# Kernel optimization log

Hardware: AMD Instinct MI355X
Metric: run time of the kernel (lower is better)

The kernel has to match this reference:

```python
import jax, jax.numpy as jnp
import numpy as np

N = 100000   # nodes
E = 1600000  # edges (avg degree 16)
IN, HID, OUT = 128, 128, 40
EPS = 1e-5   # BatchNorm1d default eps


def _lin(k, fan_in, fan_out):
    # Glorot-ish init for the linear weights
    return jax.random.normal(k, (fan_in, fan_out), jnp.float32) / np.sqrt(fan_in).astype(np.float32)


def setup_inputs() -> dict:
    key = jax.random.key(0)
    ks = jax.random.split(key, 12)
    return {
        "x": jax.random.normal(ks[0], (N, IN), jnp.float32),
        "edge_src": jax.random.randint(ks[1], (E,), 0, N, jnp.int32),
        "edge_dst": jax.random.randint(ks[2], (E,), 0, N, jnp.int32),
        # layer 0 (SAGEConv in->hid): lin_l (with bias) on aggregated neighbors, lin_r (no bias) on root
        "W_l0": _lin(ks[3], IN, HID), "b_l0": jnp.zeros((HID,), jnp.float32), "W_r0": _lin(ks[4], IN, HID),
        "g0": jnp.ones((HID,), jnp.float32), "be0": jnp.zeros((HID,), jnp.float32),
        # layer 1 (SAGEConv hid->hid)
        "W_l1": _lin(ks[5], HID, HID), "b_l1": jnp.zeros((HID,), jnp.float32), "W_r1": _lin(ks[6], HID, HID),
        "g1": jnp.ones((HID,), jnp.float32), "be1": jnp.zeros((HID,), jnp.float32),
        # layer 2 (SAGEConv hid->out)
        "W_l2": _lin(ks[7], HID, OUT), "b_l2": jnp.zeros((OUT,), jnp.float32), "W_r2": _lin(ks[8], HID, OUT),
    }


def reference(x, edge_src, edge_dst,
              W_l0, b_l0, W_r0, g0, be0,
              W_l1, b_l1, W_r1, g1, be1,
              W_l2, b_l2, W_r2):
    deg = jax.ops.segment_sum(jnp.ones((E,), x.dtype), edge_dst, num_segments=N)
    inv_deg = 1.0 / jnp.maximum(deg, 1.0)  # [N]

    def sage_conv(h, Wl, bl, Wr):
        # mean aggregation of neighbor features (gather + scatter-add), then two linears
        agg = jax.ops.segment_sum(h[edge_src], edge_dst, num_segments=N) * inv_deg[:, None]
        return agg @ Wl + bl + h @ Wr

    def bn(h, g, b):
        # BatchNorm1d in training mode: batch statistics over the node dimension
        m = h.mean(axis=0)
        v = h.var(axis=0)
        return (h - m) * (g / jnp.sqrt(v + EPS)) + b

    h = jax.nn.relu(bn(sage_conv(x, W_l0, b_l0, W_r0), g0, be0))
    h = jax.nn.relu(bn(sage_conv(h, W_l1, b_l1, W_r1), g1, be1))
    h = sage_conv(h, W_l2, b_l2, W_r2)
    return jax.nn.log_softmax(h, axis=-1)
```

## Files before the change

kernel.cpp:

```cpp
#include <hip/hip_runtime.h>
#include <hip/hip_bf16.h>

#define NNODES 100000
#define NEDGES 1600000
#define CH 128
#define OUTC 40
#define BN_EPS 1e-5f

__global__ void k_deg(const int* __restrict__ dst, int* __restrict__ deg) {
    int e = blockIdx.x * blockDim.x + threadIdx.x;
    if (e < NEDGES) atomicAdd(&deg[dst[e]], 1);
}

__global__ void k_scan1(const int* __restrict__ deg, int* __restrict__ row_ptr,
                        int* __restrict__ blkSums, float* __restrict__ inv_deg) {
    __shared__ int sd[256];
    int base = blockIdx.x * 1024 + threadIdx.x * 4;
    int t[4];
#pragma unroll
    for (int j = 0; j < 4; ++j) {
        int i = base + j;
        t[j] = (i < NNODES) ? deg[i] : 0;
        if (i < NNODES) inv_deg[i] = 1.0f / fmaxf((float)t[j], 1.0f);
    }
    int tsum = t[0] + t[1] + t[2] + t[3];
    sd[threadIdx.x] = tsum;
    __syncthreads();
    for (int off = 1; off < 256; off <<= 1) {
        int v = (threadIdx.x >= off) ? sd[threadIdx.x - off] : 0;
        __syncthreads();
        sd[threadIdx.x] += v;
        __syncthreads();
    }
    int run = sd[threadIdx.x] - tsum;
#pragma unroll
    for (int j = 0; j < 4; ++j) {
        int i = base + j;
        if (i < NNODES) row_ptr[i] = run;
        run += t[j];
    }
    if (threadIdx.x == 255) blkSums[blockIdx.x] = sd[255];
}

__global__ void k_scan2(int* blkSums, int nb) {
    if (threadIdx.x == 0 && blockIdx.x == 0) {
        int run = 0;
        for (int b = 0; b < nb; ++b) { int v = blkSums[b]; blkSums[b] = run; run += v; }
    }
}

__global__ void k_scan3(int* __restrict__ row_ptr, int* __restrict__ cursor,
                        const int* __restrict__ blkSums) {
    int i = blockIdx.x * blockDim.x + threadIdx.x;
    if (i < NNODES) {
        int v = row_ptr[i] + blkSums[i >> 10];
        row_ptr[i] = v;
        cursor[i] = v;
    }
    if (i == 0) row_ptr[NNODES] = NEDGES;
}

__global__ void k_fill(const int* __restrict__ src, const int* __restrict__ dst,
                       int* __restrict__ cursor, int* __restrict__ sorted_src) {
    int e = blockIdx.x * blockDim.x + threadIdx.x;
    if (e < NEDGES) {
        int d = dst[e];
        int pos = atomicAdd(&cursor[d], 1);
        sorted_src[pos] = src[e];
    }
}

template <bool BN>
__global__ void k_aggregate(const float* __restrict__ h, const int* __restrict__ row_ptr,
                            const int* __restrict__ sorted_src, const float* __restrict__ inv_deg,
                            const float* __restrict__ bnscale, const float* __restrict__ bnshift,
                            float* __restrict__ agg) {
    int wave = threadIdx.x >> 6;
    int lane = threadIdx.x & 63;
    int node = blockIdx.x * 4 + wave;
    if (node >= NNODES) return;
    float2 sc = make_float2(1.f, 1.f), sh = make_float2(0.f, 0.f);
    if (BN) {
        sc = *(const float2*)&bnscale[lane * 2];
        sh = *(const float2*)&bnshift[lane * 2];
    }
    int s0 = row_ptr[node], s1 = row_ptr[node + 1];
    float ax = 0.f, ay = 0.f;
    const float2* hp = (const float2*)h;
    for (int e = s0; e < s1; ++e) {
        int s = sorted_src[e];
        float2 v = hp[(size_t)s * 64 + lane];
        if (BN) {
            v.x = fmaxf(fmaf(v.x, sc.x, sh.x), 0.f);
            v.y = fmaxf(fmaf(v.y, sc.y, sh.y), 0.f);
        }
        ax += v.x; ay += v.y;
    }
    float w = inv_deg[node];
    float2* ap = (float2*)agg;
    ap[(size_t)node * 64 + lane] = make_float2(ax * w, ay * w);
}

template <int NC, int WPAD, bool BN_A, bool STATS, bool LSM>
__global__ __launch_bounds__(256) void k_gemm(
    const float* __restrict__ agg, const float* __restrict__ hin,
    const float* __restrict__ Wl, const float* __restrict__ Wr,
    const float* __restrict__ bias,
    const float* __restrict__ bnscale, const float* __restrict__ bnshift,
    float* __restrict__ z, float* __restrict__ sums) {
    constexpr int CPT = (NC + 15) / 16;
    __shared__ float A_lds[128 * 36];
    __shared__ float W_lds[32 * WPAD];
    int tid = threadIdx.x;
    int ty = tid >> 4, tx = tid & 15;
    int row0 = blockIdx.x * 128;
    float acc[8][CPT];
#pragma unroll
    for (int i = 0; i < 8; ++i)
#pragma unroll
        for (int j = 0; j < CPT; ++j) acc[i][j] = 0.f;

    for (int half = 0; half < 2; ++half) {
        const float* Asrc = half ? hin : agg;
        const float* Wsrc = half ? Wr : Wl;
        for (int kc = 0; kc < CH; kc += 32) {
            __syncthreads();
#pragma unroll
            for (int q = 0; q < 4; ++q) {
                int r = (tid >> 3) + 32 * q;
                int c = (tid & 7) << 2;
                int gr = row0 + r;
                float4 v = make_float4(0.f, 0.f, 0.f, 0.f);
                if (gr < NNODES) v = *(const float4*)&Asrc[(size_t)gr * CH + kc + c];
                if (BN_A && half == 1) {
                    float4 s4 = *(const float4*)&bnscale[kc + c];
                    float4 h4 = *(const float4*)&bnshift[kc + c];
                    v.x = fmaxf(fmaf(v.x, s4.x, h4.x), 0.f);
                    v.y = fmaxf(fmaf(v.y, s4.y, h4.y), 0.f);
                    v.z = fmaxf(fmaf(v.z, s4.z, h4.z), 0.f);
                    v.w = fmaxf(fmaf(v.w, s4.w, h4.w), 0.f);
                }
                *(float4*)&A_lds[r * 36 + c] = v;
            }
            for (int idx = tid; idx < 32 * WPAD; idx += 256) {
                int k = idx / WPAD, c = idx - k * WPAD;
                W_lds[idx] = (c < NC) ? Wsrc[(kc + k) * NC + c] : 0.f;
            }
            __syncthreads();
#pragma unroll 8
            for (int k = 0; k < 32; ++k) {
                float a[8];
#pragma unroll
                for (int i = 0; i < 8; ++i) a[i] = A_lds[(ty + 16 * i) * 36 + k];
                float wv[CPT];
#pragma unroll
                for (int j = 0; j < CPT; ++j) wv[j] = W_lds[k * WPAD + tx + 16 * j];
#pragma unroll
                for (int i = 0; i < 8; ++i)
#pragma unroll
                    for (int j = 0; j < CPT; ++j) acc[i][j] = fmaf(a[i], wv[j], acc[i][j]);
            }
        }
    }

    float bcol[CPT];
#pragma unroll
    for (int j = 0; j < CPT; ++j) {
        int c = tx + 16 * j;
        bcol[j] = (c < NC) ? bias[c] : 0.f;
    }
#pragma unroll
    for (int i = 0; i < 8; ++i)
#pragma unroll
        for (int j = 0; j < CPT; ++j) acc[i][j] += bcol[j];

    if (!LSM) {
#pragma unroll
        for (int i = 0; i < 8; ++i) {
            int gr = row0 + ty + 16 * i;
            if (gr >= NNODES) continue;
#pragma unroll
            for (int j = 0; j < CPT; ++j) {
                int c = tx + 16 * j;
                if (c < NC) z[(size_t)gr * NC + c] = acc[i][j];
            }
        }
    }

    if (STATS) {
        __shared__ float smem_s[4][128];
        __shared__ float smem_q[4][128];
        float s[CPT], q[CPT];
#pragma unroll
        for (int j = 0; j < CPT; ++j) { s[j] = 0.f; q[j] = 0.f; }
#pragma unroll
        for (int i = 0; i < 8; ++i) {
            int gr = row0 + ty + 16 * i;
            if (gr < NNODES) {
#pragma unroll
                for (int j = 0; j < CPT; ++j) {
                    float a = acc[i][j];
                    s[j] += a; q[j] += a * a;
                }
            }
        }
#pragma unroll
        for (int j = 0; j < CPT; ++j) {
            s[j] += __shfl_xor(s[j], 16); q[j] += __shfl_xor(q[j], 16);
            s[j] += __shfl_xor(s[j], 32); q[j] += __shfl_xor(q[j], 32);
        }
        int wv = tid >> 6, lane = tid & 63;
        if (lane < 16) {
#pragma unroll
            for (int j = 0; j < CPT; ++j) {
                smem_s[wv][lane + 16 * j] = s[j];
                smem_q[wv][lane + 16 * j] = q[j];
            }
        }
        __syncthreads();
        if (tid < NC) {
            atomicAdd(&sums[tid], smem_s[0][tid] + smem_s[1][tid] + smem_s[2][tid] + smem_s[3][tid]);
        } else if (tid >= 128 && tid < 128 + NC) {
            int c = tid - 128;
            atomicAdd(&sums[128 + c], smem_q[0][c] + smem_q[1][c] + smem_q[2][c] + smem_q[3][c]);
        }
    }

    if (LSM) {
#pragma unroll
        for (int i = 0; i < 8; ++i) {
            int gr = row0 + ty + 16 * i;
            if (gr >= NNODES) continue;
            float m = -INFINITY;
#pragma unroll
            for (int j = 0; j < CPT; ++j)
                if (tx + 16 * j < NC) m = fmaxf(m, acc[i][j]);
            m = fmaxf(m, __shfl_xor(m, 1));
            m = fmaxf(m, __shfl_xor(m, 2));
            m = fmaxf(m, __shfl_xor(m, 4));
            m = fmaxf(m, __shfl_xor(m, 8));
            float se = 0.f;
#pragma unroll
            for (int j = 0; j < CPT; ++j)
                if (tx + 16 * j < NC) se += expf(acc[i][j] - m);
            se += __shfl_xor(se, 1);
            se += __shfl_xor(se, 2);
            se += __shfl_xor(se, 4);
            se += __shfl_xor(se, 8);
            float lse = m + logf(se);
#pragma unroll
            for (int j = 0; j < CPT; ++j) {
                int c = tx + 16 * j;
                if (c < NC) z[(size_t)gr * NC + c] = acc[i][j] - lse;
            }
        }
    }
}

__global__ void k_bn_finalize(const float* __restrict__ sums, const float* __restrict__ g,
                              const float* __restrict__ be, float* __restrict__ scale,
                              float* __restrict__ shift) {
    int c = threadIdx.x;
    if (c < CH) {
        float mean = sums[c] * (1.0f / NNODES);
        float var = sums[128 + c] * (1.0f / NNODES) - mean * mean;
        float sc = g[c] * rsqrtf(var + BN_EPS);
        scale[c] = sc;
        shift[c] = be[c] - mean * sc;
    }
}

extern "C" void kernel_launch(void* const* d_in, const int* in_sizes, int n_in,
                              void* d_out, int out_size, void* d_ws, size_t ws_size,
                              hipStream_t stream) {
    const float* x   = (const float*)d_in[0];
    const int* esrc  = (const int*)d_in[1];
    const int* edst  = (const int*)d_in[2];
    const float* W_l0 = (const float*)d_in[3];
    const float* b_l0 = (const float*)d_in[4];
    const float* W_r0 = (const float*)d_in[5];
    const float* g0   = (const float*)d_in[6];
    const float* be0  = (const float*)d_in[7];
    const float* W_l1 = (const float*)d_in[8];
    const float* b_l1 = (const float*)d_in[9];
    const float* W_r1 = (const float*)d_in[10];
    const float* g1   = (const float*)d_in[11];
    const float* be1  = (const float*)d_in[12];
    const float* W_l2 = (const float*)d_in[13];
    const float* b_l2 = (const float*)d_in[14];
    const float* W_r2 = (const float*)d_in[15];
    float* out = (float*)d_out;

    char* w = (char*)d_ws;
    size_t o = 0;
    auto nxt = [&](size_t b) { void* p = w + o; o = (o + b + 511) & ~(size_t)511; return p; };
    int* deg      = (int*)nxt((size_t)NNODES * 4);
    int* row_ptr  = (int*)nxt((size_t)(NNODES + 1) * 4);
    int* cursor   = (int*)nxt((size_t)NNODES * 4);
    float* invdeg = (float*)nxt((size_t)NNODES * 4);
    int* blkSums  = (int*)nxt(128 * 4);
    float* sums   = (float*)nxt(512 * 4);
    float* scsh   = (float*)nxt(512 * 4);
    int* sorted   = (int*)nxt((size_t)NEDGES * 4);
    float* agg    = (float*)nxt((size_t)NNODES * CH * 4);
    float* z0     = (float*)nxt((size_t)NNODES * CH * 4);
    float* z1     = (float*)nxt((size_t)NNODES * CH * 4);
    float* sums0 = sums, *sums1 = sums + 256;
    float* scale0 = scsh, *shift0 = scsh + 128, *scale1 = scsh + 256, *shift1 = scsh + 384;

    hipMemsetAsync(deg, 0, (size_t)NNODES * 4, stream);
    hipMemsetAsync(sums, 0, 512 * 4, stream);

    const int EB = (NEDGES + 255) / 256;
    const int SCAN_B = (NNODES + 1023) / 1024;
    const int NB = (NNODES + 255) / 256;
    const int AGG_B = (NNODES + 3) / 4;
    const int GEMM_B = (NNODES + 127) / 128;

    k_deg<<<EB, 256, 0, stream>>>(edst, deg);
    k_scan1<<<SCAN_B, 256, 0, stream>>>(deg, row_ptr, blkSums, invdeg);
    k_scan2<<<1, 64, 0, stream>>>(blkSums, SCAN_B);
    k_scan3<<<NB, 256, 0, stream>>>(row_ptr, cursor, blkSums);
    k_fill<<<EB, 256, 0, stream>>>(esrc, edst, cursor, sorted);

    k_aggregate<false><<<AGG_B, 256, 0, stream>>>(x, row_ptr, sorted, invdeg,
                                                  nullptr, nullptr, agg);
    k_gemm<128, 132, false, true, false><<<GEMM_B, 256, 0, stream>>>(
        agg, x, W_l0, W_r0, b_l0, nullptr, nullptr, z0, sums0);
    k_bn_finalize<<<1, 128, 0, stream>>>(sums0, g0, be0, scale0, shift0);

    k_aggregate<true><<<AGG_B, 256, 0, stream>>>(z0, row_ptr, sorted, invdeg,
                                                 scale0, shift0, agg);
    k_gemm<128, 132, true, true, false><<<GEMM_B, 256, 0, stream>>>(
        agg, z0, W_l1, W_r1, b_l1, scale0, shift0, z1, sums1);
    k_bn_finalize<<<1, 128, 0, stream>>>(sums1, g1, be1, scale1, shift1);

    k_aggregate<true><<<AGG_B, 256, 0, stream>>>(z1, row_ptr, sorted, invdeg,
                                                 scale1, shift1, agg);
    k_gemm<40, 48, true, false, true><<<GEMM_B, 256, 0, stream>>>(
        agg, z1, W_l2, W_r2, b_l2, scale1, shift1, out, nullptr);
}
```

Baseline: 1.258 ms.

## Transform-then-aggregate: apply linear before mean aggregation, fuse combine with log-softmax

```diff
diff --git a/kernel.cpp b/kernel.cpp
--- a/kernel.cpp
+++ b/kernel.cpp
@@ -70,59 +70,29 @@
     }
 }
 
-template <bool BN>
-__global__ void k_aggregate(const float* __restrict__ h, const int* __restrict__ row_ptr,
-                            const int* __restrict__ sorted_src, const float* __restrict__ inv_deg,
-                            const float* __restrict__ bnscale, const float* __restrict__ bnshift,
-                            float* __restrict__ agg) {
-    int wave = threadIdx.x >> 6;
-    int lane = threadIdx.x & 63;
-    int node = blockIdx.x * 4 + wave;
-    if (node >= NNODES) return;
-    float2 sc = make_float2(1.f, 1.f), sh = make_float2(0.f, 0.f);
-    if (BN) {
-        sc = *(const float2*)&bnscale[lane * 2];
-        sh = *(const float2*)&bnshift[lane * 2];
-    }
-    int s0 = row_ptr[node], s1 = row_ptr[node + 1];
-    float ax = 0.f, ay = 0.f;
-    const float2* hp = (const float2*)h;
-    for (int e = s0; e < s1; ++e) {
-        int s = sorted_src[e];
-        float2 v = hp[(size_t)s * 64 + lane];
-        if (BN) {
-            v.x = fmaxf(fmaf(v.x, sc.x, sh.x), 0.f);
-            v.y = fmaxf(fmaf(v.y, sc.y, sh.y), 0.f);
-        }
-        ax += v.x; ay += v.y;
-    }
-    float w = inv_deg[node];
-    float2* ap = (float2*)agg;
-    ap[(size_t)node * 64 + lane] = make_float2(ax * w, ay * w);
-}
-
-template <int NC, int WPAD, bool BN_A, bool STATS, bool LSM>
-__global__ __launch_bounds__(256) void k_gemm(
-    const float* __restrict__ agg, const float* __restrict__ hin,
+template <int NC, int WP, bool BN_A>
+__global__ __launch_bounds__(256) void k_gemm2(
+    const float* __restrict__ h,
     const float* __restrict__ Wl, const float* __restrict__ Wr,
     const float* __restrict__ bias,
     const float* __restrict__ bnscale, const float* __restrict__ bnshift,
-    float* __restrict__ z, float* __restrict__ sums) {
-    constexpr int CPT = (NC + 15) / 16;
+    float* __restrict__ yl, float* __restrict__ yr) {
+    constexpr int NG = (NC == 128) ? 2 : 1;
+    constexpr int WSLOTS = NC / 4;
     __shared__ float A_lds[128 * 36];
-    __shared__ float W_lds[32 * WPAD];
+    __shared__ float W_lds[32 * WP];
     int tid = threadIdx.x;
     int ty = tid >> 4, tx = tid & 15;
     int row0 = blockIdx.x * 128;
-    float acc[8][CPT];
-#pragma unroll
-    for (int i = 0; i < 8; ++i)
-#pragma unroll
-        for (int j = 0; j < CPT; ++j) acc[i][j] = 0.f;
 
     for (int half = 0; half < 2; ++half) {
-        const float* Asrc = half ? hin : agg;
-        const float* Wsrc = half ? Wr : Wl;
+        const float* W = half ? Wr : Wl;
+        float acc[8][NG * 4];
+#pragma unroll
+        for (int i = 0; i < 8; ++i)
+#pragma unroll
+            for (int j = 0; j < NG * 4; ++j) acc[i][j] = 0.f;
+
         for (int kc = 0; kc < CH; kc += 32) {
             __syncthreads();
 #pragma unroll
@@ -131,8 +101,8 @@
                 int c = (tid & 7) << 2;
                 int gr = row0 + r;
                 float4 v = make_float4(0.f, 0.f, 0.f, 0.f);
-                if (gr < NNODES) v = *(const float4*)&Asrc[(size_t)gr * CH + kc + c];
-                if (BN_A && half == 1) {
+                if (gr < NNODES) v = *(const float4*)&h[(size_t)gr * CH + kc + c];
+                if (BN_A) {
                     float4 s4 = *(const float4*)&bnscale[kc + c];
                     float4 h4 = *(const float4*)&bnshift[kc + c];
                     v.x = fmaxf(fmaf(v.x, s4.x, h4.x), 0.f);
@@ -142,118 +112,160 @@
                 }
                 *(float4*)&A_lds[r * 36 + c] = v;
             }
-            for (int idx = tid; idx < 32 * WPAD; idx += 256) {
-                int k = idx / WPAD, c = idx - k * WPAD;
-                W_lds[idx] = (c < NC) ? Wsrc[(kc + k) * NC + c] : 0.f;
+            for (int idx = tid; idx < 32 * WSLOTS; idx += 256) {
+                int k = idx / WSLOTS, s = idx - k * WSLOTS;
+                *(float4*)&W_lds[k * WP + s * 4] = *(const float4*)&W[(size_t)(kc + k) * NC + s * 4];
             }
             __syncthreads();
-#pragma unroll 8
-            for (int k = 0; k < 32; ++k) {
-                float a[8];
-#pragma unroll
-                for (int i = 0; i < 8; ++i) a[i] = A_lds[(ty + 16 * i) * 36 + k];
-                float wv[CPT];
-#pragma unroll
-                for (int j = 0; j < CPT; ++j) wv[j] = W_lds[k * WPAD + tx + 16 * j];
+#pragma unroll
+            for (int k4 = 0; k4 < 32; k4 += 4) {
+                float4 a4[8];
 #pragma unroll
                 for (int i = 0; i < 8; ++i)
-#pragma unroll
-                    for (int j = 0; j < CPT; ++j) acc[i][j] = fmaf(a[i], wv[j], acc[i][j]);
+                    a4[i] = *(const float4*)&A_lds[(ty + 16 * i) * 36 + k4];
+#pragma unroll
+                for (int kk = 0; kk < 4; ++kk) {
+                    float4 w0 = *(const float4*)&W_lds[(k4 + kk) * WP + tx * 4];
+                    float4 w1;
+                    if (NG == 2) w1 = *(const float4*)&W_lds[(k4 + kk) * WP + 64 + tx * 4];
+#pragma unroll
+                    for (int i = 0; i < 8; ++i) {
+                        float av = (&a4[i].x)[kk];
+                        acc[i][0] = fmaf(av, w0.x, acc[i][0]);
+                        acc[i][1] = fmaf(av, w0.y, acc[i][1]);
+                        acc[i][2] = fmaf(av, w0.z, acc[i][2]);
+                        acc[i][3] = fmaf(av, w0.w, acc[i][3]);
+                        if (NG == 2) {
+                            acc[i][4] = fmaf(av, w1.x, acc[i][4]);
+                            acc[i][5] = fmaf(av, w1.y, acc[i][5]);
+                            acc[i][6] = fmaf(av, w1.z, acc[i][6]);
+                            acc[i][7] = fmaf(av, w1.w, acc[i][7]);
+                        }
+                    }
+                }
             }
         }
-    }
-
-    float bcol[CPT];
-#pragma unroll
-    for (int j = 0; j < CPT; ++j) {
-        int c = tx + 16 * j;
-        bcol[j] = (c < NC) ? bias[c] : 0.f;
-    }
-#pragma unroll
-    for (int i = 0; i < 8; ++i)
-#pragma unroll
-        for (int j = 0; j < CPT; ++j) acc[i][j] += bcol[j];
-
-    if (!LSM) {
+        float* Y = half ? yr : yl;
+        bool colok = (NC != 40) || (tx < 10);
+        float4 b0 = make_float4(0.f, 0.f, 0.f, 0.f), b1 = b0;
+        if (half == 1 && colok) {
+            b0 = *(const float4*)&bias[tx * 4];
+            if (NG == 2) b1 = *(const float4*)&bias[64 + tx * 4];
+        }
 #pragma unroll
         for (int i = 0; i < 8; ++i) {
             int gr = row0 + ty + 16 * i;
-            if (gr >= NNODES) continue;
-#pragma unroll
-            for (int j = 0; j < CPT; ++j) {
-                int c = tx + 16 * j;
-                if (c < NC) z[(size_t)gr * NC + c] = acc[i][j];
+            if (gr >= NNODES || !colok) continue;
+            float4 v0 = make_float4(acc[i][0] + b0.x, acc[i][1] + b0.y,
+                                    acc[i][2] + b0.z, acc[i][3] + b0.w);
+            *(float4*)&Y[(size_t)gr * NC + tx * 4] = v0;
+            if (NG == 2) {
+                float4 v1 = make_float4(acc[i][4] + b1.x, acc[i][5] + b1.y,
+                                        acc[i][6] + b1.z, acc[i][7] + b1.w);
+                *(float4*)&Y[(size_t)gr * NC + 64 + tx * 4] = v1;
             }
         }
     }
-
-    if (STATS) {
-        __shared__ float smem_s[4][128];
-        __shared__ float smem_q[4][128];
-        float s[CPT], q[CPT];
-#pragma unroll
-        for (int j = 0; j < CPT; ++j) { s[j] = 0.f; q[j] = 0.f; }
-#pragma unroll
-        for (int i = 0; i < 8; ++i) {
-            int gr = row0 + ty + 16 * i;
-            if (gr < NNODES) {
-#pragma unroll
-                for (int j = 0; j < CPT; ++j) {
-                    float a = acc[i][j];
-                    s[j] += a; q[j] += a * a;
-                }
-            }
-        }
-#pragma unroll
-        for (int j = 0; j < CPT; ++j) {
-            s[j] += __shfl_xor(s[j], 16); q[j] += __shfl_xor(q[j], 16);
-            s[j] += __shfl_xor(s[j], 32); q[j] += __shfl_xor(q[j], 32);
-        }
-        int wv = tid >> 6, lane = tid & 63;
-        if (lane < 16) {
-#pragma unroll
-            for (int j = 0; j < CPT; ++j) {
-                smem_s[wv][lane + 16 * j] = s[j];
-                smem_q[wv][lane + 16 * j] = q[j];
-            }
-        }
-        __syncthreads();
-        if (tid < NC) {
-            atomicAdd(&sums[tid], smem_s[0][tid] + smem_s[1][tid] + smem_s[2][tid] + smem_s[3][tid]);
-        } else if (tid >= 128 && tid < 128 + NC) {
-            int c = tid - 128;
-            atomicAdd(&sums[128 + c], smem_q[0][c] + smem_q[1][c] + smem_q[2][c] + smem_q[3][c]);
-        }
-    }
-
-    if (LSM) {
-#pragma unroll
-        for (int i = 0; i < 8; ++i) {
-            int gr = row0 + ty + 16 * i;
-            if (gr >= NNODES) continue;
-            float m = -INFINITY;
-#pragma unroll
-            for (int j = 0; j < CPT; ++j)
-                if (tx + 16 * j < NC) m = fmaxf(m, acc[i][j]);
-            m = fmaxf(m, __shfl_xor(m, 1));
-            m = fmaxf(m, __shfl_xor(m, 2));
-            m = fmaxf(m, __shfl_xor(m, 4));
-            m = fmaxf(m, __shfl_xor(m, 8));
-            float se = 0.f;
-#pragma unroll
-            for (int j = 0; j < CPT; ++j)
-                if (tx + 16 * j < NC) se += expf(acc[i][j] - m);
-            se += __shfl_xor(se, 1);
-            se += __shfl_xor(se, 2);
-            se += __shfl_xor(se, 4);
-            se += __shfl_xor(se, 8);
-            float lse = m + logf(se);
-#pragma unroll
-            for (int j = 0; j < CPT; ++j) {
-                int c = tx + 16 * j;
-                if (c < NC) z[(size_t)gr * NC + c] = acc[i][j] - lse;
-            }
-        }
+}
+
+__global__ void k_combine128(const float* __restrict__ yl, const int* __restrict__ row_ptr,
+                             const int* __restrict__ sorted_src, const float* __restrict__ inv_deg,
+                             float* __restrict__ z) {
+    int wave = threadIdx.x >> 6, lane = threadIdx.x & 63;
+    int node = blockIdx.x * 4 + wave;
+    if (node >= NNODES) return;
+    int s0 = row_ptr[node], s1 = row_ptr[node + 1];
+    const float2* Y = (const float2*)yl;
+    float ax0 = 0.f, ay0 = 0.f, ax1 = 0.f, ay1 = 0.f;
+    float ax2 = 0.f, ay2 = 0.f, ax3 = 0.f, ay3 = 0.f;
+    int e = s0;
+    for (; e + 4 <= s1; e += 4) {
+        int i0 = sorted_src[e], i1 = sorted_src[e + 1];
+        int i2 = sorted_src[e + 2], i3 = sorted_src[e + 3];
+        float2 v0 = Y[(size_t)i0 * 64 + lane];
+        float2 v1 = Y[(size_t)i1 * 64 + lane];
+        float2 v2 = Y[(size_t)i2 * 64 + lane];
+        float2 v3 = Y[(size_t)i3 * 64 + lane];
+        ax0 += v0.x; ay0 += v0.y; ax1 += v1.x; ay1 += v1.y;
+        ax2 += v2.x; ay2 += v2.y; ax3 += v3.x; ay3 += v3.y;
+    }
+    for (; e < s1; ++e) {
+        int i = sorted_src[e];
+        float2 v = Y[(size_t)i * 64 + lane];
+        ax0 += v.x; ay0 += v.y;
+    }
+    float w = inv_deg[node];
+    float2* Z = (float2*)z;
+    float2 r = Z[(size_t)node * 64 + lane];
+    r.x += (ax0 + ax1 + ax2 + ax3) * w;
+    r.y += (ay0 + ay1 + ay2 + ay3) * w;
+    Z[(size_t)node * 64 + lane] = r;
+}
+
+__global__ void k_combine40_lsm(const float* __restrict__ yl, const float* __restrict__ yr,
+                                const int* __restrict__ row_ptr, const int* __restrict__ sorted_src,
+                                const float* __restrict__ inv_deg, float* __restrict__ out) {
+    int wave = threadIdx.x >> 6, lane = threadIdx.x & 63;
+    int node = blockIdx.x * 4 + wave;
+    if (node >= NNODES) return;
+    bool act = lane < 20;
+    int s0 = row_ptr[node], s1 = row_ptr[node + 1];
+    float ax0 = 0.f, ay0 = 0.f, ax1 = 0.f, ay1 = 0.f;
+    float ax2 = 0.f, ay2 = 0.f, ax3 = 0.f, ay3 = 0.f;
+    int e = s0;
+    for (; e + 4 <= s1; e += 4) {
+        int i0 = sorted_src[e], i1 = sorted_src[e + 1];
+        int i2 = sorted_src[e + 2], i3 = sorted_src[e + 3];
+        if (act) {
+            float2 v0 = *(const float2*)&yl[(size_t)i0 * OUTC + lane * 2];
+            float2 v1 = *(const float2*)&yl[(size_t)i1 * OUTC + lane * 2];
+            float2 v2 = *(const float2*)&yl[(size_t)i2 * OUTC + lane * 2];
+            float2 v3 = *(const float2*)&yl[(size_t)i3 * OUTC + lane * 2];
+            ax0 += v0.x; ay0 += v0.y; ax1 += v1.x; ay1 += v1.y;
+            ax2 += v2.x; ay2 += v2.y; ax3 += v3.x; ay3 += v3.y;
+        }
+    }
+    for (; e < s1; ++e) {
+        int i = sorted_src[e];
+        if (act) {
+            float2 v = *(const float2*)&yl[(size_t)i * OUTC + lane * 2];
+            ax0 += v.x; ay0 += v.y;
+        }
+    }
+    float zx = 0.f, zy = 0.f;
+    if (act) {
+        float w = inv_deg[node];
+        float2 r = *(const float2*)&yr[(size_t)node * OUTC + lane * 2];
+        zx = (ax0 + ax1 + ax2 + ax3) * w + r.x;
+        zy = (ay0 + ay1 + ay2 + ay3) * w + r.y;
+    }
+    float m = act ? fmaxf(zx, zy) : -INFINITY;
+#pragma unroll
+    for (int off = 1; off <= 16; off <<= 1) m = fmaxf(m, __shfl_xor(m, off));
+    float se = act ? (expf(zx - m) + expf(zy - m)) : 0.f;
+#pragma unroll
+    for (int off = 1; off <= 16; off <<= 1) se += __shfl_xor(se, off);
+    float lse = m + logf(se);
+    if (act) {
+        float2 o = make_float2(zx - lse, zy - lse);
+        *(float2*)&out[(size_t)node * OUTC + lane * 2] = o;
+    }
+}
+
+__global__ void k_stats(const float* __restrict__ h, float* __restrict__ sums) {
+    __shared__ float ls[256], ls2[256];
+    int c = threadIdx.x & 127;
+    int half = threadIdx.x >> 7;
+    float s = 0.f, s2 = 0.f;
+    for (int r = blockIdx.x * 2 + half; r < NNODES; r += gridDim.x * 2) {
+        float v = h[(size_t)r * CH + c];
+        s += v; s2 += v * v;
+    }
+    ls[threadIdx.x] = s; ls2[threadIdx.x] = s2;
+    __syncthreads();
+    if (half == 0) {
+        atomicAdd(&sums[c], ls[c] + ls[c + 128]);
+        atomicAdd(&sums[CH + c], ls2[c] + ls2[c + 128]);
     }
 }
 
@@ -302,9 +314,9 @@
     float* sums   = (float*)nxt(512 * 4);
     float* scsh   = (float*)nxt(512 * 4);
     int* sorted   = (int*)nxt((size_t)NEDGES * 4);
-    float* agg    = (float*)nxt((size_t)NNODES * CH * 4);
-    float* z0     = (float*)nxt((size_t)NNODES * CH * 4);
-    float* z1     = (float*)nxt((size_t)NNODES * CH * 4);
+    float* ylbuf  = (float*)nxt((size_t)NNODES * CH * 4);
+    float* zA     = (float*)nxt((size_t)NNODES * CH * 4);
+    float* zB     = (float*)nxt((size_t)NNODES * CH * 4);
     float* sums0 = sums, *sums1 = sums + 256;
     float* scale0 = scsh, *shift0 = scsh + 128, *scale1 = scsh + 256, *shift1 = scsh + 384;
 
@@ -314,7 +326,7 @@
     const int EB = (NEDGES + 255) / 256;
     const int SCAN_B = (NNODES + 1023) / 1024;
     const int NB = (NNODES + 255) / 256;
-    const int AGG_B = (NNODES + 3) / 4;
+    const int COMB_B = (NNODES + 3) / 4;
     const int GEMM_B = (NNODES + 127) / 128;
 
     k_deg<<<EB, 256, 0, stream>>>(edst, deg);
@@ -323,20 +335,19 @@
     k_scan3<<<NB, 256, 0, stream>>>(row_ptr, cursor, blkSums);
     k_fill<<<EB, 256, 0, stream>>>(esrc, edst, cursor, sorted);
 
-    k_aggregate<false><<<AGG_B, 256, 0, stream>>>(x, row_ptr, sorted, invdeg,
-                                                  nullptr, nullptr, agg);
-    k_gemm<128, 132, false, true, false><<<GEMM_B, 256, 0, stream>>>(
-        agg, x, W_l0, W_r0, b_l0, nullptr, nullptr, z0, sums0);
+    k_gemm2<128, 132, false><<<GEMM_B, 256, 0, stream>>>(
+        x, W_l0, W_r0, b_l0, nullptr, nullptr, ylbuf, zA);
+    k_combine128<<<COMB_B, 256, 0, stream>>>(ylbuf, row_ptr, sorted, invdeg, zA);
+    k_stats<<<256, 256, 0, stream>>>(zA, sums0);
     k_bn_finalize<<<1, 128, 0, stream>>>(sums0, g0, be0, scale0, shift0);
 
-    k_aggregate<true><<<AGG_B, 256, 0, stream>>>(z0, row_ptr, sorted, invdeg,
-                                                 scale0, shift0, agg);
-    k_gemm<128, 132, true, true, false><<<GEMM_B, 256, 0, stream>>>(
-        agg, z0, W_l1, W_r1, b_l1, scale0, shift0, z1, sums1);
+    k_gemm2<128, 132, true><<<GEMM_B, 256, 0, stream>>>(
+        zA, W_l1, W_r1, b_l1, scale0, shift0, ylbuf, zB);
+    k_combine128<<<COMB_B, 256, 0, stream>>>(ylbuf, row_ptr, sorted, invdeg, zB);
+    k_stats<<<256, 256, 0, stream>>>(zB, sums1);
     k_bn_finalize<<<1, 128, 0, stream>>>(sums1, g1, be1, scale1, shift1);
 
-    k_aggregate<true><<<AGG_B, 256, 0, stream>>>(z1, row_ptr, sorted, invdeg,
-                                                 scale1, shift1, agg);
-    k_gemm<40, 48, true, false, true><<<GEMM_B, 256, 0, stream>>>(
-        agg, z1, W_l2, W_r2, b_l2, scale1, shift1, out, nullptr);
-}
+    k_gemm2<40, 64, true><<<GEMM_B, 256, 0, stream>>>(
+        zB, W_l2, W_r2, b_l2, scale1, shift1, ylbuf, zA);
+    k_combine40_lsm<<<COMB_B, 256, 0, stream>>>(ylbuf, zA, row_ptr, sorted, invdeg, out);
+}
```

Measured after the change: 1.050 ms. 16.5% less time.
